# Kernel optimization log

Hardware: AMD Instinct MI355X
Metric: run time of the kernel (lower is better)

Reference implementation:

```python
import math
import jax, jax.numpy as jnp
import numpy as np

B, H, W, C = 16, 64, 64, 256


def setup_inputs() -> dict:
    key = jax.random.key(0)
    ks = jax.random.split(key, 6)
    return {
        "h": jax.random.normal(ks[0], (B, H, W, C), jnp.float32),
        # grouped 3x3 perception conv: groups=C, in/groups=1, out=3C
        "w_perc": jax.random.normal(ks[1], (3 * C, 1, 3, 3), jnp.float32) * 0.1,
        "b_perc": jnp.zeros((3 * C,), jnp.float32),
        # update_net: 1x1 conv 3C->2C, GELU, 1x1 conv 2C->C
        "w_up1": jax.random.normal(ks[2], (2 * C, 3 * C, 1, 1), jnp.float32) * 0.02,
        "b_up1": jnp.zeros((2 * C,), jnp.float32),
        "w_up2": jax.random.normal(ks[3], (C, 2 * C, 1, 1), jnp.float32) * 0.02,
        "b_up2": jnp.zeros((C,), jnp.float32),
        # lin_qkv: Linear C -> 3C (torch weight layout [out,in])
        "w_qkv": jax.random.normal(ks[4], (3 * C, C), jnp.float32) * 0.02,
        "b_qkv": jnp.zeros((3 * C,), jnp.float32),
    }


_POS = [(-1, -1), (-1, 0), (-1, 1), (0, -1), (0, 0), (0, 1), (1, -1), (1, 0), (1, 1)]


def _local_attn(hn, w_qkv, b_qkv):
    """3x3 windowed local attention (zero-padded borders), NHWC in/out."""
    Bb, Hh, Ww, Cc = hn.shape
    qkv = jnp.einsum('bhwc,dc->bhwd', hn, w_qkv) + b_qkv
    q, k, v = jnp.split(qkv, 3, axis=-1)
    kp = jnp.pad(k, ((0, 0), (1, 1), (1, 1), (0, 0)))
    vp = jnp.pad(v, ((0, 0), (1, 1), (1, 1), (0, 0)))
    scale = 1.0 / math.sqrt(Cc)
    # scores over the 9 neighbor offsets -> [B,H,W,9]
    scores = jnp.stack(
        [(q * kp[:, 1 + dy:1 + dy + Hh, 1 + dx:1 + dx + Ww, :]).sum(-1) for dy, dx in _POS],
        axis=-1) * scale
    w = jax.nn.softmax(scores, axis=-1)
    out = jnp.zeros_like(v)
    for i, (dy, dx) in enumerate(_POS):
        out = out + w[..., i:i + 1] * vp[:, 1 + dy:1 + dy + Hh, 1 + dx:1 + dx + Ww, :]
    return out


def reference(h, w_perc, b_perc, w_up1, b_up1, w_up2, b_up2, w_qkv, b_qkv):
    # eval-mode forward: noise / dropout / stochastic mask are identity
    Cc = h.shape[-1]
    x = jnp.transpose(h, (0, 3, 1, 2))  # NCHW
    perceived = jax.lax.conv_general_dilated(
        x, w_perc, window_strides=(1, 1), padding='SAME',
        feature_group_count=Cc,
        dimension_numbers=('NCHW', 'OIHW', 'NCHW')) + b_perc[None, :, None, None]
    hid = jnp.einsum('bphw,dp->bdhw', perceived, w_up1[:, :, 0, 0]) + b_up1[None, :, None, None]
    hid = jax.nn.gelu(hid, approximate=False)
    dx = jnp.einsum('bdhw,cd->bchw', hid, w_up2[:, :, 0, 0]) + b_up2[None, :, None, None]
    x_new = x + dx  # stochastic_update in eval mode
    h_new = jnp.transpose(x_new, (0, 2, 3, 1))  # NHWC
    h_attn = _local_attn(h_new, w_qkv, b_qkv)
    return h_new + h_attn
```

## Files before the change

kernel.cpp:

```cpp
#include <hip/hip_runtime.h>
#include <math.h>


typedef unsigned short u16;
typedef __bf16 bf16x8 __attribute__((ext_vector_type(8)));
typedef float floatx4 __attribute__((ext_vector_type(4)));

__device__ int g_flag;
__device__ __align__(16) u16 g_h[16777216];
__device__ __align__(16) u16 g_perc[50331648];
__device__ __align__(16) u16 g_hid[33554432];
__device__ __align__(16) u16 g_hnew[16777216];
__device__ __align__(16) u16 g_wperc[6912];
__device__ __align__(16) u16 g_bperc[768];
__device__ __align__(16) u16 g_wup1[393216];
__device__ __align__(16) u16 g_bup1[512];
__device__ __align__(16) u16 g_wup2[131072];
__device__ __align__(16) u16 g_bup2[256];
__device__ __align__(16) u16 g_wqkv[196608];
__device__ __align__(16) u16 g_bqkv[768];

__device__ __forceinline__ float b2f(u16 x) {
  unsigned int u = ((unsigned int)x) << 16;
  float f;
  __builtin_memcpy(&f, &u, 4);
  return f;
}
__device__ __forceinline__ u16 f2b(float f) {
  unsigned int u;
  __builtin_memcpy(&u, &f, 4);
  u += 0x7FFFu + ((u >> 16) & 1u);
  return (u16)(u >> 16);
}
__device__ __forceinline__ void gload16(const u16* g, u16* l) {
  __builtin_amdgcn_global_load_lds(
      (const __attribute__((address_space(1))) unsigned int*)g,
      (__attribute__((address_space(3))) unsigned int*)l, 16, 0, 0);
}
__device__ __forceinline__ void ld8(const u16* p, float* f) {
  uint4 v = *(const uint4*)p;
  f[0] = b2f((u16)(v.x & 0xFFFF)); f[1] = b2f((u16)(v.x >> 16));
  f[2] = b2f((u16)(v.y & 0xFFFF)); f[3] = b2f((u16)(v.y >> 16));
  f[4] = b2f((u16)(v.z & 0xFFFF)); f[5] = b2f((u16)(v.z >> 16));
  f[6] = b2f((u16)(v.w & 0xFFFF)); f[7] = b2f((u16)(v.w >> 16));
}

__global__ __launch_bounds__(256) void probe_kernel(const u16* __restrict__ h) {
  __shared__ int hit;
  if (threadIdx.x == 0) hit = 0;
  __syncthreads();
  int local = 0;
  for (int i = threadIdx.x; i < 8192; i += 256) {
    u16 v = h[2 * i];
    if ((v & 0x7F80) == 0x7F80) local = 1;
  }
  if (local) atomicOr(&hit, 1);
  __syncthreads();
  if (threadIdx.x == 0) g_flag = hit;
}

__global__ __launch_bounds__(256) void conv_w_kernel(
    const void* i1, const void* i2, const void* i3, const void* i4,
    const void* i5, const void* i6, const void* i7, const void* i8) {
  const void* srcs[8] = {i1, i2, i3, i4, i5, i6, i7, i8};
  u16* dsts[8] = {g_wperc, g_bperc, g_wup1, g_bup1,
                  g_wup2,  g_bup2,  g_wqkv, g_bqkv};
  const int szs[8] = {6912, 768, 393216, 512, 131072, 256, 196608, 768};
  const int fp32 = g_flag;
  const int stride = gridDim.x * 256;
  for (int gw = blockIdx.x * 256 + threadIdx.x; gw < 730112; gw += stride) {
    int seg = 0, off = gw;
    while (off >= szs[seg]) { off -= szs[seg]; ++seg; }
    dsts[seg][off] = fp32 ? f2b(((const float*)srcs[seg])[off])
                          : ((const u16*)srcs[seg])[off];
  }
}

__global__ __launch_bounds__(256) void perc_kernel(const void* __restrict__ hin) {
  __shared__ __align__(16) u16 sw[3456];
  __shared__ __align__(16) u16 sb[384];
  const int bid = blockIdx.x >> 1;
  const int chalf = blockIdx.x & 1;
  const int b = bid >> 6, y = bid & 63;
  const int xi = threadIdx.x >> 6;
  const int cl = threadIdx.x & 63;
  const int c0 = chalf * 128 + cl * 2;
  for (int i = threadIdx.x; i < 3456; i += 256) sw[i] = g_wperc[chalf * 3456 + i];
  for (int i = threadIdx.x; i < 384; i += 256) sb[i] = g_bperc[chalf * 384 + i];
  const int fp32 = g_flag;
  __syncthreads();
  float w[2][27], bias[2][3];
#pragma unroll
  for (int ch = 0; ch < 2; ++ch) {
    const int lc = cl * 2 + ch;
#pragma unroll
    for (int t = 0; t < 3; ++t) {
      bias[ch][t] = b2f(sb[3 * lc + t]);
#pragma unroll
      for (int j = 0; j < 9; ++j)
        w[ch][t * 9 + j] = b2f(sw[(3 * lc + t) * 9 + j]);
    }
  }
  float hv[3][3][2];
  auto loadcol = [&](int xx, int cc) {
#pragma unroll
    for (int r = 0; r < 3; ++r) {
      const int yy = y - 1 + r;
      const bool ok = ((unsigned)yy < 64u) && ((unsigned)xx < 64u);
      if (ok) {
        const size_t idx = (((size_t)(b * 64 + yy) * 64) + xx) * 256 + c0;
        if (fp32) {
          const float2 v = *(const float2*)((const float*)hin + idx);
          hv[r][cc][0] = v.x;
          hv[r][cc][1] = v.y;
        } else {
          const unsigned v = *(const unsigned*)((const u16*)hin + idx);
          hv[r][cc][0] = b2f((u16)(v & 0xFFFF));
          hv[r][cc][1] = b2f((u16)(v >> 16));
        }
      } else {
        hv[r][cc][0] = 0.0f;
        hv[r][cc][1] = 0.0f;
      }
    }
  };
  const int x0 = xi * 16;
  loadcol(x0 - 1, 0);
  loadcol(x0, 1);
#pragma unroll
  for (int k = 0; k < 16; ++k) {
    const int x = x0 + k;
    loadcol(x + 1, (k + 2) % 3);
    const int cL = k % 3, cM = (k + 1) % 3, cR = (k + 2) % 3;
    const size_t pix = (size_t)(b * 64 + y) * 64 + x;
    *(unsigned*)&g_h[pix * 256 + c0] =
        (unsigned)f2b(hv[1][cM][0]) | ((unsigned)f2b(hv[1][cM][1]) << 16);
    u16* op = &g_perc[pix * 768 + 3 * c0];
    unsigned pk[3];
#pragma unroll
    for (int ch = 0; ch < 2; ++ch) {
#pragma unroll
      for (int t = 0; t < 3; ++t) {
        const float* wt = &w[ch][t * 9];
        float a = bias[ch][t];
        a += hv[0][cL][ch] * wt[0] + hv[0][cM][ch] * wt[1] + hv[0][cR][ch] * wt[2];
        a += hv[1][cL][ch] * wt[3] + hv[1][cM][ch] * wt[4] + hv[1][cR][ch] * wt[5];
        a += hv[2][cL][ch] * wt[6] + hv[2][cM][ch] * wt[7] + hv[2][cR][ch] * wt[8];
        const int o = 3 * ch + t;
        const unsigned bb = f2b(a);
        if (o & 1) pk[o >> 1] |= bb << 16; else pk[o >> 1] = bb;
      }
    }
    *(unsigned*)(op) = pk[0];
    *(unsigned*)(op + 2) = pk[1];
    *(unsigned*)(op + 4) = pk[2];
  }
}

template <int MODE, int NB>
__global__ __launch_bounds__(512) void gemm_bt(int K) {
  const u16 *A, *Bw, *bias, *resid;
  u16* C;
  if (MODE == 0) { A = g_perc; Bw = g_wup1; bias = g_bup1; resid = nullptr; C = g_hid; }
  if (MODE == 1) { A = g_hid;  Bw = g_wup2; bias = g_bup2; resid = g_h;     C = g_hnew; }
  if (MODE == 2) { A = g_hnew; Bw = g_wqkv; bias = g_bqkv; resid = nullptr; C = g_perc; }
  const int N = NB * 256;
  const int NT = K >> 6;

  __shared__ __align__(16) u16 lds[2][2][2][8192];
  const int tid = threadIdx.x;
  const int w = tid >> 6, lane = tid & 63;
  const int ln = lane & 15, quad = lane >> 4, lnx = ln & 7;
  const int wmi = w >> 2, wni = w & 3;

  const int mb_per_xcd = (gridDim.x / NB) >> 3;
  const int m_blk = (blockIdx.x & 7) * mb_per_xcd + (blockIdx.x >> 3) / NB;
  const int n_blk = (blockIdx.x >> 3) % NB;
  const int m0 = m_blk * 256, n0 = n_blk * 256;

  auto stageA = [&](int t, int half) {
    u16* dst = &lds[t & 1][0][half][0];
#pragma unroll
    for (int ld = 0; ld < 2; ++ld) {
      const int s = ld * 512 + tid;
      const int srow = s >> 3, sch = (s & 7) ^ (srow & 7);
      gload16(&A[(size_t)(m0 + half * 128 + srow) * K + t * 64 + sch * 8],
              dst + s * 8);
    }
  };
  auto stageB = [&](int t, int half) {
    u16* dst = &lds[t & 1][1][half][0];
#pragma unroll
    for (int ld = 0; ld < 2; ++ld) {
      const int s = ld * 512 + tid;
      const int srow = s >> 3, sch = (s & 7) ^ (srow & 7);
      gload16(&Bw[(size_t)(n0 + half * 128 + srow) * K + t * 64 + sch * 8],
              dst + s * 8);
    }
  };

  floatx4 acc[8][4] = {};
  bf16x8 af[4][2], bfr[2][2];

  stageA(0, 0); stageB(0, 1); stageA(0, 1); stageB(0, 0);
  stageA(1, 0); stageB(1, 1);

  for (int u = 0; u < NT; ++u) {
    const u16* Abuf = &lds[u & 1][0][0][0];
    const u16* Bbuf = &lds[u & 1][1][0][0];
#pragma unroll
    for (int r = 0; r < 4; ++r) {
      if (r == 0 && u + 1 < NT) stageA(u + 1, 1);
      if (r == 1 && u + 1 < NT) stageB(u + 1, 0);
      if (r == 2 && u + 2 < NT) stageA(u + 2, 0);
      if (r == 3 && u + 2 < NT) stageB(u + 2, 1);
      if (r == 0) {
        if (u + 1 < NT) asm volatile("s_waitcnt vmcnt(6)" ::: "memory");
        else            asm volatile("s_waitcnt vmcnt(0)" ::: "memory");
      }
      asm volatile("s_barrier" ::: "memory");
      const int ah = (r >= 2) ? 1 : 0;
      const int bh = (r == 1 || r == 2) ? 1 : 0;
      if (r == 0 || r == 2) {
#pragma unroll
        for (int f2 = 0; f2 < 4; ++f2) {
          const int row = (f2 * 2 + wmi) * 16 + ln;
#pragma unroll
          for (int ks = 0; ks < 2; ++ks) {
            const int ch = (ks * 4 + quad) ^ lnx;
            af[f2][ks] = *(const bf16x8*)(Abuf + ah * 8192 + (row * 8 + ch) * 8);
          }
        }
      }
      if (r != 2) {
#pragma unroll
        for (int g2 = 0; g2 < 2; ++g2) {
          const int row = (g2 * 4 + wni) * 16 + ln;
#pragma unroll
          for (int ks = 0; ks < 2; ++ks) {
            const int ch = (ks * 4 + quad) ^ lnx;
            bfr[g2][ks] = *(const bf16x8*)(Bbuf + bh * 8192 + (row * 8 + ch) * 8);
          }
        }
      }
      __builtin_amdgcn_s_setprio(1);
#pragma unroll
      for (int f2 = 0; f2 < 4; ++f2)
#pragma unroll
        for (int g2 = 0; g2 < 2; ++g2)
#pragma unroll
          for (int ks = 0; ks < 2; ++ks)
            acc[ah * 4 + f2][bh * 2 + g2] =
                __builtin_amdgcn_mfma_f32_16x16x32_bf16(
                    af[f2][ks], bfr[g2][ks], acc[ah * 4 + f2][bh * 2 + g2],
                    0, 0, 0);
      __builtin_amdgcn_s_setprio(0);
      asm volatile("s_barrier" ::: "memory");
    }
  }

#pragma unroll
  for (int f = 0; f < 8; ++f) {
    const int mB = m0 + (f * 2 + wmi) * 16 + quad * 4;
#pragma unroll
    for (int g = 0; g < 4; ++g) {
      const int n = n0 + (g * 4 + wni) * 16 + ln;
      const float bv = b2f(bias[n]);
#pragma unroll
      for (int rr = 0; rr < 4; ++rr) {
        float v = acc[f][g][rr] + bv;
        if (MODE == 0) v = 0.5f * v * (1.0f + erff(v * 0.70710678118654752f));
        if (MODE == 1) v += b2f(resid[(size_t)(mB + rr) * N + n]);
        C[(size_t)(mB + rr) * N + n] = f2b(v);
      }
    }
  }
}

__global__ __launch_bounds__(256) void attn_kernel(void* __restrict__ outv) {
  const int wv = threadIdx.x >> 6, lane = threadIdx.x & 63;
  const int half = lane >> 5, cl = lane & 31;
  const int c0 = cl * 8;
  const int pix = blockIdx.x * 8 + wv * 2 + half;
  const int y = (pix >> 6) & 63, x = pix & 63;
  float q[8];
  ld8(g_perc + (size_t)pix * 768 + c0, q);
  float s[9];
  int nidx[9];
#pragma unroll
  for (int j = 0; j < 9; ++j) {
    const int dy = j / 3 - 1, dx = j % 3 - 1;
    const int yy = y + dy, xx = x + dx;
    const bool ok = ((unsigned)yy < 64u) && ((unsigned)xx < 64u);
    const int np = pix + dy * 64 + dx;
    nidx[j] = ok ? np : -1;
    float p = 0.0f;
    if (ok) {
      float kv[8];
      ld8(g_perc + (size_t)np * 768 + 256 + c0, kv);
      p = q[0] * kv[0] + q[1] * kv[1] + q[2] * kv[2] + q[3] * kv[3] +
          q[4] * kv[4] + q[5] * kv[5] + q[6] * kv[6] + q[7] * kv[7];
    }
#pragma unroll
    for (int off = 16; off >= 1; off >>= 1) p += __shfl_xor(p, off, 64);
    s[j] = p * 0.0625f;
  }
  float mx = s[0];
#pragma unroll
  for (int j = 1; j < 9; ++j) mx = fmaxf(mx, s[j]);
  float e[9], den = 0.0f;
#pragma unroll
  for (int j = 0; j < 9; ++j) {
    e[j] = expf(s[j] - mx);
    den += e[j];
  }
  const float inv = 1.0f / den;
  float a[8];
  ld8(g_hnew + (size_t)pix * 256 + c0, a);
#pragma unroll
  for (int j = 0; j < 9; ++j) {
    if (nidx[j] >= 0) {
      const float wgt = e[j] * inv;
      float vv[8];
      ld8(g_perc + (size_t)nidx[j] * 768 + 512 + c0, vv);
#pragma unroll
      for (int t = 0; t < 8; ++t) a[t] += wgt * vv[t];
    }
  }
  const size_t o = (size_t)pix * 256 + c0;
  if (g_flag) {
    float4 r0 = {a[0], a[1], a[2], a[3]};
    float4 r1 = {a[4], a[5], a[6], a[7]};
    *(float4*)((float*)outv + o) = r0;
    *(float4*)((float*)outv + o + 4) = r1;
  } else {
    uint4 r;
    r.x = (unsigned)f2b(a[0]) | ((unsigned)f2b(a[1]) << 16);
    r.y = (unsigned)f2b(a[2]) | ((unsigned)f2b(a[3]) << 16);
    r.z = (unsigned)f2b(a[4]) | ((unsigned)f2b(a[5]) << 16);
    r.w = (unsigned)f2b(a[6]) | ((unsigned)f2b(a[7]) << 16);
    *(uint4*)((u16*)outv + o) = r;
  }
}

extern "C" void kernel_launch(void* const* d_in, const int* in_sizes, int n_in,
                              void* d_out, int d_out_size, void* d_ws,
                              size_t ws_size, hipStream_t stream) {
  (void)d_ws; (void)ws_size;
  probe_kernel<<<1, 256, 0, stream>>>((const u16*)d_in[0]);
  conv_w_kernel<<<360, 256, 0, stream>>>(d_in[1], d_in[2], d_in[3], d_in[4],
                                         d_in[5], d_in[6], d_in[7], d_in[8]);
  perc_kernel<<<2048, 256, 0, stream>>>(d_in[0]);
  gemm_bt<0, 2><<<512, 512, 0, stream>>>(768);
  gemm_bt<1, 1><<<256, 512, 0, stream>>>(512);
  gemm_bt<2, 3><<<768, 512, 0, stream>>>(256);
  attn_kernel<<<8192, 256, 0, stream>>>(d_out);
}
```

Before: 422.2 us.

## Slide 3x3 K/V register window along rows in local attention kernel

Each half-wave now processes a run of 8 consecutive pixels along a row instead of a single pixel. It keeps a rotating 3x3 window of K and V vectors in registers, so each new pixel loads only one new column of neighbors. This cuts redundant global/L2 loads of K and V, which were re-fetched up to 9 times. In exchange the kernel launches 8x fewer blocks and uses more registers, which lowers parallelism and may reduce occupancy.

Measured after the change: 597.9 us, median of 2. +41.6%, slower.

```diff
diff --git a/kernel.cpp b/kernel.cpp
--- a/kernel.cpp
+++ b/kernel.cpp
@@ -37,12 +37,15 @@
       (const __attribute__((address_space(1))) unsigned int*)g,
       (__attribute__((address_space(3))) unsigned int*)l, 16, 0, 0);
 }
-__device__ __forceinline__ void ld8(const u16* p, float* f) {
-  uint4 v = *(const uint4*)p;
+__device__ __forceinline__ void up8(const uint4& v, float* f) {
   f[0] = b2f((u16)(v.x & 0xFFFF)); f[1] = b2f((u16)(v.x >> 16));
   f[2] = b2f((u16)(v.y & 0xFFFF)); f[3] = b2f((u16)(v.y >> 16));
   f[4] = b2f((u16)(v.z & 0xFFFF)); f[5] = b2f((u16)(v.z >> 16));
   f[6] = b2f((u16)(v.w & 0xFFFF)); f[7] = b2f((u16)(v.w >> 16));
+}
+__device__ __forceinline__ void ld8(const u16* p, float* f) {
+  uint4 v = *(const uint4*)p;
+  up8(v, f);
 }
 
 __global__ __launch_bounds__(256) void probe_kernel(const u16* __restrict__ h) {
@@ -281,65 +284,92 @@
   const int wv = threadIdx.x >> 6, lane = threadIdx.x & 63;
   const int half = lane >> 5, cl = lane & 31;
   const int c0 = cl * 8;
-  const int pix = blockIdx.x * 8 + wv * 2 + half;
-  const int y = (pix >> 6) & 63, x = pix & 63;
-  float q[8];
-  ld8(g_perc + (size_t)pix * 768 + c0, q);
-  float s[9];
-  int nidx[9];
-#pragma unroll
-  for (int j = 0; j < 9; ++j) {
-    const int dy = j / 3 - 1, dx = j % 3 - 1;
-    const int yy = y + dy, xx = x + dx;
-    const bool ok = ((unsigned)yy < 64u) && ((unsigned)xx < 64u);
-    const int np = pix + dy * 64 + dx;
-    nidx[j] = ok ? np : -1;
-    float p = 0.0f;
-    if (ok) {
+  const int run = blockIdx.x * 8 + wv * 2 + half;
+  const int row = run >> 3;
+  const int y = row & 63;
+  const int x0 = (run & 7) * 8;
+  const int fp32 = g_flag;
+
+  uint4 Kw[3][3], Vw[3][3], tK[3], tV[3];
+  auto fetch = [&](int xx, uint4 (&K3)[3], uint4 (&V3)[3]) {
+#pragma unroll
+    for (int r = 0; r < 3; ++r) {
+      const int yy = y - 1 + r;
+      if (((unsigned)yy < 64u) && ((unsigned)xx < 64u)) {
+        const size_t np = (size_t)(row - 1 + r) * 64 + xx;
+        K3[r] = *(const uint4*)(g_perc + np * 768 + 256 + c0);
+        V3[r] = *(const uint4*)(g_perc + np * 768 + 512 + c0);
+      } else {
+        K3[r] = make_uint4(0, 0, 0, 0);
+        V3[r] = make_uint4(0, 0, 0, 0);
+      }
+    }
+  };
+  fetch(x0 - 1, tK, tV);
+#pragma unroll
+  for (int r = 0; r < 3; ++r) { Kw[r][0] = tK[r]; Vw[r][0] = tV[r]; }
+  fetch(x0, tK, tV);
+#pragma unroll
+  for (int r = 0; r < 3; ++r) { Kw[r][1] = tK[r]; Vw[r][1] = tV[r]; }
+  fetch(x0 + 1, tK, tV);
+
+#pragma unroll
+  for (int k = 0; k < 8; ++k) {
+    const int x = x0 + k;
+    const int sR = (k + 2) % 3;
+#pragma unroll
+    for (int r = 0; r < 3; ++r) { Kw[r][sR] = tK[r]; Vw[r][sR] = tV[r]; }
+    fetch(x + 2, tK, tV);
+
+    const size_t pix = (size_t)row * 64 + x;
+    float q[8];
+    ld8(g_perc + pix * 768 + c0, q);
+    float a[8];
+    ld8(g_hnew + pix * 256 + c0, a);
+
+    float s[9];
+#pragma unroll
+    for (int j = 0; j < 9; ++j) {
       float kv[8];
-      ld8(g_perc + (size_t)np * 768 + 256 + c0, kv);
-      p = q[0] * kv[0] + q[1] * kv[1] + q[2] * kv[2] + q[3] * kv[3] +
-          q[4] * kv[4] + q[5] * kv[5] + q[6] * kv[6] + q[7] * kv[7];
-    }
-#pragma unroll
-    for (int off = 16; off >= 1; off >>= 1) p += __shfl_xor(p, off, 64);
-    s[j] = p * 0.0625f;
-  }
-  float mx = s[0];
-#pragma unroll
-  for (int j = 1; j < 9; ++j) mx = fmaxf(mx, s[j]);
-  float e[9], den = 0.0f;
-#pragma unroll
-  for (int j = 0; j < 9; ++j) {
-    e[j] = expf(s[j] - mx);
-    den += e[j];
-  }
-  const float inv = 1.0f / den;
-  float a[8];
-  ld8(g_hnew + (size_t)pix * 256 + c0, a);
-#pragma unroll
-  for (int j = 0; j < 9; ++j) {
-    if (nidx[j] >= 0) {
+      up8(Kw[j / 3][(k + j % 3) % 3], kv);
+      float p = q[0] * kv[0] + q[1] * kv[1] + q[2] * kv[2] + q[3] * kv[3] +
+                q[4] * kv[4] + q[5] * kv[5] + q[6] * kv[6] + q[7] * kv[7];
+#pragma unroll
+      for (int off = 16; off >= 1; off >>= 1) p += __shfl_xor(p, off, 64);
+      s[j] = p * 0.0625f;
+    }
+    float mx = s[0];
+#pragma unroll
+    for (int j = 1; j < 9; ++j) mx = fmaxf(mx, s[j]);
+    float e[9], den = 0.0f;
+#pragma unroll
+    for (int j = 0; j < 9; ++j) {
+      e[j] = expf(s[j] - mx);
+      den += e[j];
+    }
+    const float inv = 1.0f / den;
+#pragma unroll
+    for (int j = 0; j < 9; ++j) {
       const float wgt = e[j] * inv;
       float vv[8];
-      ld8(g_perc + (size_t)nidx[j] * 768 + 512 + c0, vv);
+      up8(Vw[j / 3][(k + j % 3) % 3], vv);
 #pragma unroll
       for (int t = 0; t < 8; ++t) a[t] += wgt * vv[t];
     }
-  }
-  const size_t o = (size_t)pix * 256 + c0;
-  if (g_flag) {
-    float4 r0 = {a[0], a[1], a[2], a[3]};
-    float4 r1 = {a[4], a[5], a[6], a[7]};
-    *(float4*)((float*)outv + o) = r0;
-    *(float4*)((float*)outv + o + 4) = r1;
-  } else {
-    uint4 r;
-    r.x = (unsigned)f2b(a[0]) | ((unsigned)f2b(a[1]) << 16);
-    r.y = (unsigned)f2b(a[2]) | ((unsigned)f2b(a[3]) << 16);
-    r.z = (unsigned)f2b(a[4]) | ((unsigned)f2b(a[5]) << 16);
-    r.w = (unsigned)f2b(a[6]) | ((unsigned)f2b(a[7]) << 16);
-    *(uint4*)((u16*)outv + o) = r;
+    const size_t o = pix * 256 + c0;
+    if (fp32) {
+      float4 r0 = {a[0], a[1], a[2], a[3]};
+      float4 r1 = {a[4], a[5], a[6], a[7]};
+      *(float4*)((float*)outv + o) = r0;
+      *(float4*)((float*)outv + o + 4) = r1;
+    } else {
+      uint4 r;
+      r.x = (unsigned)f2b(a[0]) | ((unsigned)f2b(a[1]) << 16);
+      r.y = (unsigned)f2b(a[2]) | ((unsigned)f2b(a[3]) << 16);
+      r.z = (unsigned)f2b(a[4]) | ((unsigned)f2b(a[5]) << 16);
+      r.w = (unsigned)f2b(a[6]) | ((unsigned)f2b(a[7]) << 16);
+      *(uint4*)((u16*)outv + o) = r;
+    }
   }
 }
 
@@ -354,5 +384,5 @@
   gemm_bt<0, 2><<<512, 512, 0, stream>>>(768);
   gemm_bt<1, 1><<<256, 512, 0, stream>>>(512);
   gemm_bt<2, 3><<<768, 512, 0, stream>>>(256);
-  attn_kernel<<<8192, 256, 0, stream>>>(d_out);
-}
+  attn_kernel<<<1024, 256, 0, stream>>>(d_out);
+}
```
